# Kernel optimization log

Hardware: AMD Instinct MI355X
Metric: run time of the kernel (lower is better)

The kernel has to match this reference:

```python
import jax, jax.numpy as jnp
import numpy as np
from jax import lax

GAMMA = 1.0
BIG = 1e8  # finite stand-in for +inf boundary (exp(-BIG/gamma) underflows to 0, so math is exact)


def _soft_dtw(x, y, gamma):
    """Soft-DTW values R[N, M] per batch element. x: (B,N,D), y: (B,M,D)."""
    B, N, _ = x.shape
    M = y.shape[1]
    # pairwise squared-L2 cost matrix (B, N, M)
    x2 = jnp.sum(x * x, axis=-1)  # (B, N)
    y2 = jnp.sum(y * y, axis=-1)  # (B, M)
    D = x2[:, :, None] + y2[:, None, :] - 2.0 * jnp.einsum('bnd,bmd->bnm', x, y)

    i = jnp.arange(N + 1)
    # R matrix diagonals, indexed by i (row); diag d holds R[i, d-i].
    r0 = jnp.full((B, N + 1), BIG, dtype=x.dtype).at[:, 0].set(0.0)  # d=0: R[0,0]=0
    r1 = jnp.full((B, N + 1), BIG, dtype=x.dtype)                    # d=1: boundaries

    def step(carry, d):
        r2, r1 = carry  # diagonals d-2 and d-1
        j = d - i
        valid = (i >= 1) & (i <= N) & (j >= 1) & (j <= M)
        ii = jnp.clip(i - 1, 0, N - 1)
        jj = jnp.clip(j - 1, 0, M - 1)
        cost = D[:, ii, jj]                                      # (B, N+1)
        pad = jnp.full((B, 1), BIG, dtype=x.dtype)
        r1_up = jnp.concatenate([pad, r1[:, :-1]], axis=1)       # R[i-1, j]
        r2_up = jnp.concatenate([pad, r2[:, :-1]], axis=1)       # R[i-1, j-1]
        stacked = jnp.stack([r1_up, r1, r2_up], axis=0)
        smin = -gamma * jax.scipy.special.logsumexp(-stacked / gamma, axis=0)
        new = jnp.where(valid[None, :], cost + smin, BIG)
        return (r1, new), None

    (_, r_last), _ = lax.scan(step, (r0, r1), jnp.arange(2, N + M + 1))
    return r_last[:, N]  # R[N, M] per batch


def setup_inputs() -> dict:
    key = jax.random.key(0)
    k1, k2 = jax.random.split(key)
    B, T, D = 64, 512, 64
    inputs = jax.random.normal(k1, (B, T, D), dtype=jnp.float32)
    targets = jax.random.normal(k2, (B, T, D), dtype=jnp.float32)
    return {"inputs": inputs, "targets": targets}


def reference(inputs, targets):
    # forward: mean over batch of soft-DTW(gamma=1.0) with pairwise squared-L2 cost
    return jnp.mean(_soft_dtw(inputs, targets, GAMMA))
```

## Files before the change

kernel.cpp:

```cpp
#include <hip/hip_runtime.h>

#define BIGF 100000000.0f
#define LOG2E 1.4426950408889634f
#define LN2f 0.6931471805599453f
constexpr int BATCH = 64;
constexpr int T = 512;
constexpr int DIMS = 64;

constexpr int SS = 12;
constexpr int RING = 24;
constexpr int PADF = 512;
constexpr int NSS = 86;

#if __has_builtin(__builtin_amdgcn_exp2f)
#define EXP2F(x) __builtin_amdgcn_exp2f(x)
#else
#define EXP2F(x) __expf((x) * LN2f)
#endif
#if __has_builtin(__builtin_amdgcn_logf)
#define LOG2F(x) __builtin_amdgcn_logf(x)
#else
#define LOG2F(x) (__logf(x) * LOG2E)
#endif

#if __has_builtin(__builtin_amdgcn_update_dpp)
#define ROTL1(x) __int_as_float(__builtin_amdgcn_update_dpp(               \
    0, __float_as_int(x), 0x13C, 0xF, 0xF, 1))
#else
#define ROTL1(x) __int_as_float(__builtin_amdgcn_ds_bpermute(              \
    rot_addr, __float_as_int(x)))
#endif

__global__ __launch_bounds__(256) void pairdist_diag_kernel(
    const float* __restrict__ x, const float* __restrict__ y,
    float* __restrict__ D) {
  int bid = blockIdx.x;
  int b = bid >> 6;
  int tile = bid & 63;
  int n0 = (tile >> 3) << 6;
  int m0 = (tile & 7) << 6;

  __shared__ float xs[64][65];
  __shared__ float ys[64][65];
  __shared__ float stage[64][66];
  __shared__ float x2s[64], y2s[64];

  const float* xb = x + ((size_t)b * T + n0) * DIMS;
  const float* yb = y + ((size_t)b * T + m0) * DIMS;
  int tid = threadIdx.x;

  for (int e = tid; e < 64 * 64; e += 256) {
    int r = e >> 6, c = e & 63;
    xs[r][c] = xb[(size_t)r * DIMS + c];
    ys[r][c] = yb[(size_t)r * DIMS + c];
  }
  __syncthreads();

  if (tid < 64) {
    float s = 0.f;
    #pragma unroll
    for (int k = 0; k < 64; ++k) { float v = xs[tid][k]; s += v * v; }
    x2s[tid] = s;
  } else if (tid < 128) {
    int r = tid - 64;
    float s = 0.f;
    #pragma unroll
    for (int k = 0; k < 64; ++k) { float v = ys[r][k]; s += v * v; }
    y2s[r] = s;
  }
  __syncthreads();

  int tr = tid >> 4, tc = tid & 15;
  int r0 = tr * 4, c0 = tc * 4;
  float acc[4][4] = {};
  #pragma unroll 8
  for (int k = 0; k < 64; ++k) {
    float a0 = xs[r0 + 0][k], a1 = xs[r0 + 1][k];
    float a2 = xs[r0 + 2][k], a3 = xs[r0 + 3][k];
    float b0 = ys[c0 + 0][k], b1 = ys[c0 + 1][k];
    float b2 = ys[c0 + 2][k], b3 = ys[c0 + 3][k];
    acc[0][0] += a0 * b0; acc[0][1] += a0 * b1; acc[0][2] += a0 * b2; acc[0][3] += a0 * b3;
    acc[1][0] += a1 * b0; acc[1][1] += a1 * b1; acc[1][2] += a1 * b2; acc[1][3] += a1 * b3;
    acc[2][0] += a2 * b0; acc[2][1] += a2 * b1; acc[2][2] += a2 * b2; acc[2][3] += a2 * b3;
    acc[3][0] += a3 * b0; acc[3][1] += a3 * b1; acc[3][2] += a3 * b2; acc[3][3] += a3 * b3;
  }

  #pragma unroll
  for (int r = 0; r < 4; ++r) {
    float xn = x2s[r0 + r];
    #pragma unroll
    for (int c = 0; c < 4; ++c)
      stage[r0 + r][c0 + c] = (xn + y2s[c0 + c] - 2.f * acc[r][c]) * LOG2E;
  }
  __syncthreads();

  float* Dp = D + (size_t)b * (T * T);
  int p = tid & 63;
  int sub = __builtin_amdgcn_readfirstlane(tid >> 6);
  int ldsoff = 65 * p;
  #pragma unroll 1
  for (int t = sub; t <= 126; t += 4) {
    int rlo = (t > 63) ? t - 63 : 0;
    int rhi = (t < 63) ? t : 63;
    int d = n0 + m0 + t + 2;
    int lo = (d <= T + 1) ? 1 : d - T;
    int off = (d <= T + 1) ? (((d - 2) * (d - 1)) >> 1)
                           : (T * T - (((2 * T + 1 - d) * (2 * T + 2 - d)) >> 1));
    int r = rlo + p;
    if (r <= rhi) {
      float v = ((const float*)stage)[ldsoff + 65 * rlo + t];
      Dp[off + (n0 + r + 1 - lo)] = v;
    }
  }
}

#define ISSUE(BANK, slot_, dd_)                                               \
  {                                                                           \
    const int di = (dd_);                                                     \
    if (di <= 2 * T) {                                                        \
      const int lo_ = (di <= T + 1) ? 1 : di - T;                             \
      const float* sp = &lds[PADF + (slot_) * T + 1 - lo_];                   \
      _Pragma("unroll")                                                       \
      for (int k = 0; k < 8; ++k) BANK[k] = sp[(k << 6) + lane];              \
    }                                                                         \
  }

#define COMPUTE(dd_, RP2, RP1, ROUT, BANK)                                    \
  {                                                                           \
    const int d_ = (dd_);                                                     \
    if (d_ <= 2 * T) {                                                        \
      const float dzero = (d_ == 2) ? 0.0f : BIGF;                            \
      float rot1[8], rot2[8];                                                 \
      _Pragma("unroll")                                                       \
      for (int k = 0; k < 8; ++k) {                                           \
        rot1[k] = ROTL1(RP1[k]);                                              \
        rot2[k] = ROTL1(RP2[k]);                                              \
      }                                                                       \
      _Pragma("unroll")                                                       \
      for (int k = 0; k < 8; ++k) {                                           \
        const int i = (k << 6) + lane + 1;                                    \
        float up, dg;                                                         \
        if (k == 0) {                                                         \
          up = (lane == 0) ? BIGF : rot1[0];                                  \
          dg = (lane == 0) ? dzero : rot2[0];                                 \
        } else {                                                              \
          up = (lane == 0) ? rot1[k - 1] : rot1[k];                           \
          dg = (lane == 0) ? rot2[k - 1] : rot2[k];                           \
        }                                                                     \
        const float lf = RP1[k];                                              \
        const float mn = fminf(fminf(up, lf), dg);                            \
        const float md = __builtin_amdgcn_fmed3f(up, lf, dg);                 \
        const float mx = fmaxf(fmaxf(up, lf), dg);                            \
        const float sv = 1.0f + EXP2F(mn - md) + EXP2F(mn - mx);              \
        const float val = BANK[k] + mn - LOG2F(sv);                           \
        const unsigned ju = (unsigned)(d_ - i - 1);                           \
        ROUT[k] = (ju < (unsigned)T) ? val : BIGF;                            \
      }                                                                       \
    }                                                                         \
  }

#define FILLSS(ss_)                                                           \
  {                                                                           \
    const int ssv = (ss_);                                                    \
    if (ssv < NSS) {                                                          \
      const int d0n = 2 + SS * ssv;                                           \
      const int halfn = (ssv & 1) * SS;                                       \
      for (int tt = wave - 1; tt < SS; tt += 4) {                             \
        const int d = d0n + tt;                                               \
        if (d <= 2 * T) {                                                     \
          const int off = (d <= T + 1)                                        \
              ? (((d - 2) * (d - 1)) >> 1)                                    \
              : (T * T - (((2 * T + 1 - d) * (2 * T + 2 - d)) >> 1));         \
          float* dst = &lds[PADF + (halfn + tt) * T];                         \
          _Pragma("unroll")                                                   \
          for (int u = 0; u < 8; ++u) {                                       \
            int gi = off + (u << 6) + lane;                                   \
            gi = (gi > T * T - 1) ? (T * T - 1) : gi;                         \
            dst[(u << 6) + lane] = Db[gi];                                    \
          }                                                                   \
        }                                                                     \
      }                                                                       \
    }                                                                         \
  }

__global__ __launch_bounds__(320, 2) void dp_ring_kernel(const float* __restrict__ D,
                                                         float* __restrict__ out) {
  const int b = blockIdx.x;
  const int tid = threadIdx.x;
  const int wave = tid >> 6;
  const int lane = tid & 63;
  const float* __restrict__ Db = D + (size_t)b * (T * T);
#if !__has_builtin(__builtin_amdgcn_update_dpp)
  const int rot_addr = ((lane + 63) & 63) << 2;
#endif

  __shared__ float lds[PADF + RING * T];

  float A[8], Bv[8], C[8], pcE[8], pcO[8];
  #pragma unroll
  for (int k = 0; k < 8; ++k) { A[k] = BIGF; Bv[k] = BIGF; C[k] = BIGF; }

  if (wave > 0) FILLSS(0)
  __syncthreads();

  #pragma unroll 1
  for (int s = 0; s < NSS; ++s) {
    if (wave == 0) {
      const int d0 = 2 + SS * s;
      const int half = (s & 1) * SS;
      ISSUE(pcE, half + 0, d0 + 0)
      ISSUE(pcO, half + 1, d0 + 1)
      COMPUTE(d0 + 0,  A, Bv, C, pcE)
      ISSUE(pcE, half + 2, d0 + 2)
      COMPUTE(d0 + 1, Bv, C,  A, pcO)
      ISSUE(pcO, half + 3, d0 + 3)
      COMPUTE(d0 + 2,  C, A, Bv, pcE)
      ISSUE(pcE, half + 4, d0 + 4)
      COMPUTE(d0 + 3,  A, Bv, C, pcO)
      ISSUE(pcO, half + 5, d0 + 5)
      COMPUTE(d0 + 4, Bv, C,  A, pcE)
      ISSUE(pcE, half + 6, d0 + 6)
      COMPUTE(d0 + 5,  C, A, Bv, pcO)
      ISSUE(pcO, half + 7, d0 + 7)
      COMPUTE(d0 + 6,  A, Bv, C, pcE)
      ISSUE(pcE, half + 8, d0 + 8)
      COMPUTE(d0 + 7, Bv, C,  A, pcO)
      ISSUE(pcO, half + 9, d0 + 9)
      COMPUTE(d0 + 8,  C, A, Bv, pcE)
      ISSUE(pcE, half + 10, d0 + 10)
      COMPUTE(d0 + 9,  A, Bv, C, pcO)
      ISSUE(pcO, half + 11, d0 + 11)
      COMPUTE(d0 + 10, Bv, C,  A, pcE)
      COMPUTE(d0 + 11,  C, A, Bv, pcO)
    } else {
      FILLSS(s + 1)
    }
    __syncthreads();
  }

  if (tid == 63) atomicAdd(out, Bv[7] * (LN2f / BATCH));
}

__global__ __launch_bounds__(512) void dp_onfly_kernel(
    const float* __restrict__ x, const float* __restrict__ y,
    float* __restrict__ out) {
  int b = blockIdx.x;
  int tid = threadIdx.x;
  int i = tid + 1;

  __shared__ float ys[T][DIMS + 1];
  __shared__ float y2s[T];
  __shared__ float rbuf[3][T + 1];

  const float* yb = y + (size_t)b * T * DIMS;
  for (int e = tid; e < T * DIMS; e += 512) {
    int r = e >> 6, c = e & 63;
    ys[r][c] = yb[e];
  }
  for (int e = tid; e < 3 * (T + 1); e += 512) ((float*)rbuf)[e] = BIGF;
  __syncthreads();
  if (tid == 0) rbuf[0][0] = 0.f;
  {
    float s = 0.f;
    #pragma unroll
    for (int k = 0; k < DIMS; ++k) { float v = ys[tid][k]; s += v * v; }
    y2s[tid] = s;
  }

  float xr[DIMS];
  float x2 = 0.f;
  const float* xb = x + ((size_t)b * T + (i - 1)) * DIMS;
  #pragma unroll
  for (int k = 0; k < DIMS; ++k) { xr[k] = xb[k]; x2 += xr[k] * xr[k]; }
  __syncthreads();

  float* rp2 = rbuf[0];
  float* rp1 = rbuf[1];
  float* rc  = rbuf[2];

  float val = BIGF;
  for (int d = 2; d <= 2 * T; ++d) {
    int j = d - i;
    bool valid = (j >= 1) && (j <= T);
    float cost = 0.f;
    if (valid) {
      float dot = 0.f;
      #pragma unroll
      for (int k = 0; k < DIMS; ++k) dot += xr[k] * ys[j - 1][k];
      cost = x2 + y2s[j - 1] - 2.f * dot;
    }
    float a = rp1[i - 1];
    float bb = rp1[i];
    float c = rp2[i - 1];
    float m = fminf(fminf(a, bb), c);
    float s = __expf(m - a) + __expf(m - bb) + __expf(m - c);
    val = valid ? (cost + m - __logf(s)) : BIGF;
    rc[i] = val;
    if (tid == 0) rc[0] = BIGF;
    __syncthreads();
    float* tmp = rp2; rp2 = rp1; rp1 = rc; rc = tmp;
  }

  if (tid == T - 1) atomicAdd(out, val * (1.0f / BATCH));
}

extern "C" void kernel_launch(void* const* d_in, const int* in_sizes, int n_in,
                              void* d_out, int out_size, void* d_ws, size_t ws_size,
                              hipStream_t stream) {
  const float* x = (const float*)d_in[0];
  const float* y = (const float*)d_in[1];
  float* out = (float*)d_out;

  hipMemsetAsync(d_out, 0, sizeof(float), stream);

  size_t needD = (size_t)BATCH * T * T * sizeof(float);
  if (ws_size >= needD) {
    float* Dw = (float*)d_ws;
    pairdist_diag_kernel<<<BATCH * 64, 256, 0, stream>>>(x, y, Dw);
    dp_ring_kernel<<<BATCH, 320, 0, stream>>>(Dw, out);
  } else {
    dp_onfly_kernel<<<BATCH, 512, 0, stream>>>(x, y, out);
  }
}
```

Before: 431.1 us.

## Skip inactive diagonal chunks and reuse rotated up-values as next diagonal term

The DP step now computes only the 64-lane chunks that intersect the valid range of each anti-diagonal, and the LDS cost loads skip the same inactive chunks. The rotated 'up' values from one step are kept and reused as the diagonal term of the next step, so only one lane rotation per chunk is needed instead of two, and the third register bank goes away. Launch bounds drop to one block per SIMD minimum, and the LDS pad is initialised to BIG. This trims work near the triangular ends and cuts cross-lane ops, at the cost of runtime-bounded predicated loops that may add branching overhead.

Result: slower. 734.7 us (+70.4%).

```diff
diff --git a/kernel.cpp b/kernel.cpp
--- a/kernel.cpp
+++ b/kernel.cpp
@@ -118,44 +118,46 @@
   {                                                                           \
     const int di = (dd_);                                                     \
     if (di <= 2 * T) {                                                        \
-      const int lo_ = (di <= T + 1) ? 1 : di - T;                             \
+      const int lo_  = (di <= T + 1) ? 1 : di - T;                            \
+      const int hi_  = (di - 1 < T) ? di - 1 : T;                             \
+      const int klo_ = (lo_ - 1) >> 6;                                        \
+      const int khi_ = (hi_ - 1) >> 6;                                        \
       const float* sp = &lds[PADF + (slot_) * T + 1 - lo_];                   \
       _Pragma("unroll")                                                       \
-      for (int k = 0; k < 8; ++k) BANK[k] = sp[(k << 6) + lane];              \
+      for (int k = 0; k < 8; ++k)                                             \
+        if (k >= klo_ && k <= khi_) BANK[k] = sp[(k << 6) + lane];            \
     }                                                                         \
   }
 
-#define COMPUTE(dd_, RP2, RP1, ROUT, BANK)                                    \
+#define STEP(dd_, RP1, ROUT, BANK, UPIN, UPOUT)                               \
   {                                                                           \
-    const int d_ = (dd_);                                                     \
-    if (d_ <= 2 * T) {                                                        \
-      const float dzero = (d_ == 2) ? 0.0f : BIGF;                            \
-      float rot1[8], rot2[8];                                                 \
+    const int dd = (dd_);                                                     \
+    if (dd <= 2 * T) {                                                        \
+      const int lo  = (dd <= T + 1) ? 1 : dd - T;                             \
+      const int hi  = (dd - 1 < T) ? dd - 1 : T;                              \
+      const int klo = (lo - 1) >> 6;                                          \
+      const int khi = (hi - 1) >> 6;                                          \
+      const int krot = (klo > 0) ? klo - 1 : 0;                               \
+      float ror1[8];                                                          \
       _Pragma("unroll")                                                       \
-      for (int k = 0; k < 8; ++k) {                                           \
-        rot1[k] = ROTL1(RP1[k]);                                              \
-        rot2[k] = ROTL1(RP2[k]);                                              \
-      }                                                                       \
+      for (int k = 0; k < 8; ++k)                                             \
+        if (k >= krot && k <= khi) ror1[k] = ROTL1(RP1[k]);                   \
       _Pragma("unroll")                                                       \
-      for (int k = 0; k < 8; ++k) {                                           \
-        const int i = (k << 6) + lane + 1;                                    \
-        float up, dg;                                                         \
-        if (k == 0) {                                                         \
-          up = (lane == 0) ? BIGF : rot1[0];                                  \
-          dg = (lane == 0) ? dzero : rot2[0];                                 \
-        } else {                                                              \
-          up = (lane == 0) ? rot1[k - 1] : rot1[k];                           \
-          dg = (lane == 0) ? rot2[k - 1] : rot2[k];                           \
+      for (int k = 0; k < 8; ++k)                                             \
+        if (k >= klo && k <= khi) {                                           \
+          UPOUT[k] = lz ? ((k == 0) ? BIGF : ror1[k - 1]) : ror1[k];          \
+          const float up  = UPOUT[k];                                         \
+          const float dgv = UPIN[k];                                          \
+          const float lf  = RP1[k];                                           \
+          const float mn  = fminf(fminf(up, lf), dgv);                        \
+          const float md  = __builtin_amdgcn_fmed3f(up, lf, dgv);             \
+          const float mx  = fmaxf(fmaxf(up, lf), dgv);                        \
+          const float sv  = 1.0f + EXP2F(mn - md) + EXP2F(mn - mx);           \
+          const float val = BANK[k] + mn - LOG2F(sv);                         \
+          const int su = dd - (k << 6) - 2;                                   \
+          const unsigned ju = (unsigned)(su - lane);                          \
+          ROUT[k] = (ju < (unsigned)T) ? val : BIGF;                          \
         }                                                                     \
-        const float lf = RP1[k];                                              \
-        const float mn = fminf(fminf(up, lf), dg);                            \
-        const float md = __builtin_amdgcn_fmed3f(up, lf, dg);                 \
-        const float mx = fmaxf(fmaxf(up, lf), dg);                            \
-        const float sv = 1.0f + EXP2F(mn - md) + EXP2F(mn - mx);              \
-        const float val = BANK[k] + mn - LOG2F(sv);                           \
-        const unsigned ju = (unsigned)(d_ - i - 1);                           \
-        ROUT[k] = (ju < (unsigned)T) ? val : BIGF;                            \
-      }                                                                       \
     }                                                                         \
   }
 
@@ -183,12 +185,13 @@
     }                                                                         \
   }
 
-__global__ __launch_bounds__(320, 2) void dp_ring_kernel(const float* __restrict__ D,
+__global__ __launch_bounds__(320, 1) void dp_ring_kernel(const float* __restrict__ D,
                                                          float* __restrict__ out) {
   const int b = blockIdx.x;
   const int tid = threadIdx.x;
   const int wave = tid >> 6;
   const int lane = tid & 63;
+  const bool lz = (lane == 0);
   const float* __restrict__ Db = D + (size_t)b * (T * T);
 #if !__has_builtin(__builtin_amdgcn_update_dpp)
   const int rot_addr = ((lane + 63) & 63) << 2;
@@ -196,9 +199,14 @@
 
   __shared__ float lds[PADF + RING * T];
 
-  float A[8], Bv[8], C[8], pcE[8], pcO[8];
+  float A[8], Bv[8], UPa[8], UPb[8], pcE[8], pcO[8];
   #pragma unroll
-  for (int k = 0; k < 8; ++k) { A[k] = BIGF; Bv[k] = BIGF; C[k] = BIGF; }
+  for (int k = 0; k < 8; ++k) {
+    A[k] = BIGF; Bv[k] = BIGF; UPa[k] = BIGF; UPb[k] = BIGF;
+  }
+  UPa[0] = lz ? 0.0f : BIGF;
+
+  for (int e = tid; e < PADF; e += 320) lds[e] = BIGF;
 
   if (wave > 0) FILLSS(0)
   __syncthreads();
@@ -210,35 +218,35 @@
       const int half = (s & 1) * SS;
       ISSUE(pcE, half + 0, d0 + 0)
       ISSUE(pcO, half + 1, d0 + 1)
-      COMPUTE(d0 + 0,  A, Bv, C, pcE)
+      STEP(d0 + 0,  Bv, A, pcE, UPa, UPb)
       ISSUE(pcE, half + 2, d0 + 2)
-      COMPUTE(d0 + 1, Bv, C,  A, pcO)
+      STEP(d0 + 1,  A, Bv, pcO, UPb, UPa)
       ISSUE(pcO, half + 3, d0 + 3)
-      COMPUTE(d0 + 2,  C, A, Bv, pcE)
+      STEP(d0 + 2,  Bv, A, pcE, UPa, UPb)
       ISSUE(pcE, half + 4, d0 + 4)
-      COMPUTE(d0 + 3,  A, Bv, C, pcO)
+      STEP(d0 + 3,  A, Bv, pcO, UPb, UPa)
       ISSUE(pcO, half + 5, d0 + 5)
-      COMPUTE(d0 + 4, Bv, C,  A, pcE)
+      STEP(d0 + 4,  Bv, A, pcE, UPa, UPb)
       ISSUE(pcE, half + 6, d0 + 6)
-      COMPUTE(d0 + 5,  C, A, Bv, pcO)
+      STEP(d0 + 5,  A, Bv, pcO, UPb, UPa)
       ISSUE(pcO, half + 7, d0 + 7)
-      COMPUTE(d0 + 6,  A, Bv, C, pcE)
+      STEP(d0 + 6,  Bv, A, pcE, UPa, UPb)
       ISSUE(pcE, half + 8, d0 + 8)
-      COMPUTE(d0 + 7, Bv, C,  A, pcO)
+      STEP(d0 + 7,  A, Bv, pcO, UPb, UPa)
       ISSUE(pcO, half + 9, d0 + 9)
-      COMPUTE(d0 + 8,  C, A, Bv, pcE)
+      STEP(d0 + 8,  Bv, A, pcE, UPa, UPb)
       ISSUE(pcE, half + 10, d0 + 10)
-      COMPUTE(d0 + 9,  A, Bv, C, pcO)
+      STEP(d0 + 9,  A, Bv, pcO, UPb, UPa)
       ISSUE(pcO, half + 11, d0 + 11)
-      COMPUTE(d0 + 10, Bv, C,  A, pcE)
-      COMPUTE(d0 + 11,  C, A, Bv, pcO)
+      STEP(d0 + 10, Bv, A, pcE, UPa, UPb)
+      STEP(d0 + 11, A, Bv, pcO, UPb, UPa)
     } else {
       FILLSS(s + 1)
     }
     __syncthreads();
   }
 
-  if (tid == 63) atomicAdd(out, Bv[7] * (LN2f / BATCH));
+  if (tid == 63) atomicAdd(out, A[7] * (LN2f / BATCH));
 }
 
 __global__ __launch_bounds__(512) void dp_onfly_kernel(
```
